# Performance work log

Hardware: AMD Instinct MI355X
Metric: run time of the kernel (lower is better)

The kernel has to match this reference:

```python
import jax, jax.numpy as jnp
import numpy as np

NUM_RBF = 16
MAX_REL = 32          # max_relative_feature
AUTOREGRESSIVE = True
D_MIN, D_MAX = 2.0, 22.0
LN_EPS = 1e-5


def setup_inputs() -> dict:
    key = jax.random.key(0)
    ks = jax.random.split(key, 6)
    B, L, A, K = 1, 1280, 14, 30
    E_feat, edge_in = 128, 16 + NUM_RBF * 4 * 10  # 656
    X = jax.random.normal(ks[0], (B, L, A, 3), dtype=jnp.float32) * 3.0
    residue_idx = jnp.tile(jnp.arange(L, dtype=jnp.int32)[None], (B, 1))
    chain_labels = jnp.zeros((B, L), dtype=jnp.int32)
    E_idx = jax.random.randint(ks[1], (B, L, K), 0, L, dtype=jnp.int32)
    atom_mask = jnp.ones((B, L, A), dtype=jnp.float32)
    W_pos = jax.random.normal(ks[2], (2 * MAX_REL + 2, 16), dtype=jnp.float32) * 0.1
    b_pos = jnp.zeros((16,), dtype=jnp.float32)
    W_edge = jax.random.normal(ks[3], (edge_in, E_feat), dtype=jnp.float32) * 0.05
    ln_gamma = jnp.ones((E_feat,), dtype=jnp.float32)
    ln_beta = jnp.zeros((E_feat,), dtype=jnp.float32)
    return {"X": X, "residue_idx": residue_idx, "chain_labels": chain_labels,
            "E_idx": E_idx, "atom_mask": atom_mask, "W_pos": W_pos,
            "b_pos": b_pos, "W_edge": W_edge, "ln_gamma": ln_gamma,
            "ln_beta": ln_beta}


def _forward(X, residue_idx, chain_labels, E_idx, W_pos, b_pos, W_edge,
             ln_gamma, ln_beta):
    B, L, A, _ = X.shape
    K = E_idx.shape[-1]
    # backbone atoms in loop order [Ca, N, C, O] -> X indices [1, 0, 2, 3]
    bb = X[:, :, jnp.array([1, 0, 2, 3]), :]          # [B, L, 4, 3]
    sc = X[:, :, 4:, :]                               # [B, L, 10, 3]
    Abb = jnp.transpose(bb, (0, 2, 1, 3))             # [B, 4, L, 3]
    Asc = jnp.transpose(sc, (0, 2, 1, 3))             # [B, 10, L, 3]
    # dense pairwise distances for all 40 (bb, sc) atom pairs: [B,4,10,L,L]
    diff = Abb[:, :, None, :, None, :] - Asc[:, None, :, None, :, :]
    D = jnp.sqrt(jnp.sum(diff * diff, axis=-1) + 1e-6)
    # gather top-k neighbor columns -> [B,4,10,L,K]
    D_nb = jnp.take_along_axis(D, E_idx[:, None, None, :, :], axis=4)
    mu = jnp.linspace(D_MIN, D_MAX, NUM_RBF, dtype=D_nb.dtype)
    sigma = (D_MAX - D_MIN) / NUM_RBF
    RBF = jnp.exp(-(((D_nb[..., None] - mu) / sigma) ** 2))  # [B,4,10,L,K,16]
    if AUTOREGRESSIVE:
        self_edges = (E_idx == jnp.arange(L, dtype=E_idx.dtype)[None, :, None])
        RBF = jnp.where(self_edges[:, None, None, :, :, None], 0.0, RBF)
    # concat order: bb outer, sc inner -> [B,L,K, 4*10*16]
    RBF_all = jnp.transpose(RBF, (0, 3, 4, 1, 2, 5)).reshape(B, L, K, 4 * 10 * NUM_RBF)
    # positional encodings
    offset = residue_idx[:, :, None] - residue_idx[:, None, :]        # [B,L,L]
    offset = jnp.take_along_axis(offset, E_idx, axis=2)               # [B,L,K]
    d_chains = (chain_labels[:, :, None] == chain_labels[:, None, :]).astype(jnp.int32)
    E_chains = jnp.take_along_axis(d_chains, E_idx, axis=2)           # [B,L,K]
    d = jnp.clip(offset + MAX_REL, 0, 2 * MAX_REL) * E_chains + (1 - E_chains) * (2 * MAX_REL + 1)
    d_onehot = jax.nn.one_hot(d, 2 * MAX_REL + 2, dtype=W_pos.dtype)  # [B,L,K,66]
    E_positional = d_onehot @ W_pos + b_pos                           # [B,L,K,16]
    E = jnp.concatenate([E_positional, RBF_all], axis=-1)             # [B,L,K,656]
    E = E @ W_edge                                                    # no bias
    # LayerNorm over last dim
    mean = jnp.mean(E, axis=-1, keepdims=True)
    var = jnp.mean((E - mean) ** 2, axis=-1, keepdims=True)
    E = (E - mean) / jnp.sqrt(var + LN_EPS) * ln_gamma + ln_beta
    return E


def reference(X, residue_idx, chain_labels, E_idx, atom_mask, W_pos, b_pos,
              W_edge, ln_gamma, ln_beta):
    E = _forward(X, residue_idx, chain_labels, E_idx, W_pos, b_pos, W_edge,
                 ln_gamma, ln_beta)
    return (E, E_idx)
```

## Files before the change

kernel.cpp:

```cpp
#include <hip/hip_runtime.h>

typedef short bf16x8 __attribute__((ext_vector_type(8)));
typedef float f32x4  __attribute__((ext_vector_type(4)));

#define L_RES 1280
#define A_ATM 14
#define K_NB  30
#define FEAT  656
#define KPAD  672
#define NKB   21
#define NCH   128
#define AF_STRIDE 680
#define EP_STRIDE 136
#define E_OUT_OFF (L_RES * K_NB * NCH)
#define NEDGE (L_RES * K_NB)

__device__ __forceinline__ ushort f2bf(float x) {
    union { float f; unsigned u; } v; v.f = x;
    unsigned r = (v.u + 0x7fffu + ((v.u >> 16) & 1u)) >> 16;
    return (ushort)r;
}

__global__ __launch_bounds__(256) void prep_kernel(const float* __restrict__ W,
                                                   const int* __restrict__ Eidx,
                                                   ushort* __restrict__ Wpack,
                                                   float* __restrict__ out) {
    const int blk = blockIdx.x;
    const int t = threadIdx.x;
    if (blk < 42) {
        int u = blk * 256 + t;
        if (u >= 84 * 128) return;
        int kbq = u >> 7;
        int n   = u & 127;
        int kb   = kbq >> 2;
        int quad = kbq & 3;
        ushort val[8];
#pragma unroll
        for (int j = 0; j < 8; j++) {
            int k = kb * 32 + quad * 8 + j;
            val[j] = (k < FEAT) ? f2bf(W[k * NCH + n]) : (ushort)0;
        }
        int lane = quad * 16 + (n & 15);
        ushort* dst = Wpack + (size_t)((((n >> 4) * NKB + kb) * 64 + lane) * 8);
        *(ulonglong2*)dst = *(const ulonglong2*)val;
    } else {
        int gid = (blk - 42) * 256 + t;
        if (gid < NEDGE) out[E_OUT_OFF + gid] = (float)Eidx[gid];
    }
}

__global__ __launch_bounds__(512) void sidechain_feat_kernel(
    const float* __restrict__ X,
    const int*   __restrict__ ridx,
    const int*   __restrict__ clab,
    const int*   __restrict__ Eidx,
    const float* __restrict__ Wpos,
    const float* __restrict__ bpos,
    const ushort* __restrict__ Wpack,
    const float* __restrict__ gamma,
    const float* __restrict__ beta,
    float* __restrict__ out)
{
    __shared__ __align__(16) ushort Af[64][AF_STRIDE];
    __shared__ float bbs[8][3];
    __shared__ float scj[2 * K_NB][10][3];
    __shared__ int   nbr[2 * K_NB];

    const int i0 = blockIdx.x * 2;
    const int t = threadIdx.x;
    const int w = t >> 6;
    const int lane = t & 63;

    if (t < 24) {
        const int perm[4] = {1, 0, 2, 3};
        int res = t / 12, r = t - res * 12;
        int a = r / 3, c = r - a * 3;
        bbs[res * 4 + a][c] = X[((i0 + res) * A_ATM + perm[a]) * 3 + c];
    }
    if (t < 2 * K_NB) nbr[t] = Eidx[i0 * K_NB + t];
    __syncthreads();

    for (int idx = t; idx < 2 * K_NB * 30; idx += 512) {
        int e = idx / 30;
        int r = idx - e * 30;
        int a = r / 3, c = r - a * 3;
        scj[e][a][c] = X[(nbr[e] * A_ATM + 4 + a) * 3 + c];
    }

    for (int idx = t; idx < 2 * K_NB * 16; idx += 512) {
        int e = idx >> 4, c = idx & 15;
        int res = i0 + (e >= K_NB);
        int row = e + (e >= K_NB ? 2 : 0);
        int j = nbr[e];
        int d;
        if (clab[res] == clab[j]) {
            int off = ridx[res] - ridx[j] + 32;
            d = off < 0 ? 0 : (off > 64 ? 64 : off);
        } else {
            d = 65;
        }
        Af[row][c] = f2bf(Wpos[d * 16 + c] + bpos[c]);
    }
    for (int idx = t; idx < 4 * AF_STRIDE; idx += 512) {
        int pr = idx / AF_STRIDE;
        int row = (pr & 1) + (pr >> 1) * 32 + 30;
        Af[row][idx % AF_STRIDE] = 0;
    }
    for (int idx = t; idx < 60 * 24; idx += 512) {
        int e = idx / 24;
        int row = e + (e >= K_NB ? 2 : 0);
        Af[row][FEAT + idx % 24] = 0;
    }
    __syncthreads();

    for (int idx = t; idx < 2 * K_NB * 40; idx += 512) {
        int e  = idx / 40;
        int p  = idx - e * 40;
        int ab = p / 10, as = p - ab * 10;
        int hi = (e >= K_NB);
        int row = e + hi * 2;
        float dx = bbs[hi * 4 + ab][0] - scj[e][as][0];
        float dy = bbs[hi * 4 + ab][1] - scj[e][as][1];
        float dz = bbs[hi * 4 + ab][2] - scj[e][as][2];
        float dist = sqrtf(dx * dx + dy * dy + dz * dz + 1e-6f);
        bool self = (nbr[e] == i0 + hi);
        unsigned* dst = (unsigned*)&Af[row][16 + p * 16];
#pragma unroll
        for (int q = 0; q < 8; q++) {
            float m0 = 2.0f + (float)(2 * q)     * (20.0f / 15.0f);
            float m1 = 2.0f + (float)(2 * q + 1) * (20.0f / 15.0f);
            float a0 = (dist - m0) * 0.8f;
            float a1 = (dist - m1) * 0.8f;
            float r0 = self ? 0.0f : __expf(-a0 * a0);
            float r1 = self ? 0.0f : __expf(-a1 * a1);
            dst[q] = (unsigned)f2bf(r0) | ((unsigned)f2bf(r1) << 16);
        }
    }
    __syncthreads();

    const int frow = lane & 15;
    const int quad = lane >> 4;
    const ushort* Ap[4];
#pragma unroll
    for (int m = 0; m < 4; m++) Ap[m] = &Af[m * 16 + frow][quad * 8];
    const ushort* Bp = Wpack + (size_t)((w * NKB) * 64 + lane) * 8;

    f32x4 acc[4];
#pragma unroll
    for (int m = 0; m < 4; m++) acc[m] = (f32x4){0.f, 0.f, 0.f, 0.f};

    bf16x8 a[4], b;
#pragma unroll
    for (int m = 0; m < 4; m++) a[m] = *(const bf16x8*)(Ap[m]);
    b = *(const bf16x8*)(Bp);

#pragma unroll
    for (int kb = 0; kb < NKB; kb++) {
        bf16x8 ca[4] = {a[0], a[1], a[2], a[3]};
        bf16x8 cb = b;
        if (kb + 1 < NKB) {
#pragma unroll
            for (int m = 0; m < 4; m++) a[m] = *(const bf16x8*)(Ap[m] + (kb + 1) * 32);
            b = *(const bf16x8*)(Bp + (size_t)(kb + 1) * 512);
        }
#pragma unroll
        for (int m = 0; m < 4; m++)
            acc[m] = __builtin_amdgcn_mfma_f32_16x16x32_bf16(ca[m], cb, acc[m], 0, 0, 0);
    }

    __syncthreads();
    float (*Epre)[EP_STRIDE] = (float (*)[EP_STRIDE])&Af[0][0];

#pragma unroll
    for (int m = 0; m < 4; m++)
#pragma unroll
        for (int r = 0; r < 4; r++)
            Epre[m * 16 + quad * 4 + r][w * 16 + frow] = acc[m][r];
    __syncthreads();

    for (int e = w; e < 2 * K_NB; e += 8) {
        int row = e + (e >= K_NB ? 2 : 0);
        float v0 = Epre[row][lane];
        float v1 = Epre[row][lane + 64];
        float s = v0 + v1;
        float q = v0 * v0 + v1 * v1;
#pragma unroll
        for (int off = 32; off > 0; off >>= 1) {
            s += __shfl_xor(s, off);
            q += __shfl_xor(q, off);
        }
        float mean = s * (1.0f / 128.0f);
        float var  = q * (1.0f / 128.0f) - mean * mean;
        float rstd = rsqrtf(var + 1e-5f);
        int eo = (e >= K_NB) ? (K_NB + e - K_NB) : e;
        float* o = out + (size_t)((i0 + (e >= K_NB)) * K_NB + (e % K_NB)) * NCH;
        (void)eo;
        o[lane]      = (v0 - mean) * rstd * gamma[lane]      + beta[lane];
        o[lane + 64] = (v1 - mean) * rstd * gamma[lane + 64] + beta[lane + 64];
    }
}

extern "C" void kernel_launch(void* const* d_in, const int* in_sizes, int n_in,
                              void* d_out, int out_size, void* d_ws, size_t ws_size,
                              hipStream_t stream) {
    const float* X     = (const float*)d_in[0];
    const int*   ridx  = (const int*)  d_in[1];
    const int*   clab  = (const int*)  d_in[2];
    const int*   Eidx  = (const int*)  d_in[3];
    const float* Wpos  = (const float*)d_in[5];
    const float* bpos  = (const float*)d_in[6];
    const float* Wedge = (const float*)d_in[7];
    const float* gamma = (const float*)d_in[8];
    const float* beta  = (const float*)d_in[9];
    float* out = (float*)d_out;

    ushort* Wpack = (ushort*)d_ws;

    prep_kernel<<<42 + (NEDGE + 255) / 256, 256, 0, stream>>>(Wedge, Eidx, Wpack, out);
    sidechain_feat_kernel<<<L_RES / 2, 512, 0, stream>>>(
        X, ridx, clab, Eidx, Wpos, bpos, Wpack, gamma, beta, out);
}
```

Measured before the change: 120.0 us.

## Build RBF A-fragments in registers per wave and drop shared-memory staging

The main kernel is restructured so that each wave owns one residue (32 padded edge rows) and computes all 128 output channels. The RBF and positional features are generated directly into MFMA A-operand registers, so the large shared-memory feature tile and most block barriers go away. LayerNorm is done in registers with 16-lane shuffles, and the E_idx copy moves from the prep kernel into the main kernel. In exchange, every wave re-reads all of the packed weights from global/L2 and holds 16 accumulators, which raises register pressure and lowers occupancy.

```diff
diff --git a/kernel.cpp b/kernel.cpp
--- a/kernel.cpp
+++ b/kernel.cpp
@@ -7,11 +7,9 @@
 #define A_ATM 14
 #define K_NB  30
 #define FEAT  656
-#define KPAD  672
 #define NKB   21
 #define NCH   128
-#define AF_STRIDE 680
-#define EP_STRIDE 136
+#define FRAG  512
 #define E_OUT_OFF (L_RES * K_NB * NCH)
 #define NEDGE (L_RES * K_NB)
 
@@ -22,34 +20,22 @@
 }
 
 __global__ __launch_bounds__(256) void prep_kernel(const float* __restrict__ W,
-                                                   const int* __restrict__ Eidx,
-                                                   ushort* __restrict__ Wpack,
-                                                   float* __restrict__ out) {
-    const int blk = blockIdx.x;
-    const int t = threadIdx.x;
-    if (blk < 42) {
-        int u = blk * 256 + t;
-        if (u >= 84 * 128) return;
-        int kbq = u >> 7;
-        int n   = u & 127;
-        int kb   = kbq >> 2;
-        int quad = kbq & 3;
-        ushort val[8];
-#pragma unroll
-        for (int j = 0; j < 8; j++) {
-            int k = kb * 32 + quad * 8 + j;
-            val[j] = (k < FEAT) ? f2bf(W[k * NCH + n]) : (ushort)0;
-        }
-        int lane = quad * 16 + (n & 15);
-        ushort* dst = Wpack + (size_t)((((n >> 4) * NKB + kb) * 64 + lane) * 8);
-        *(ulonglong2*)dst = *(const ulonglong2*)val;
-    } else {
-        int gid = (blk - 42) * 256 + t;
-        if (gid < NEDGE) out[E_OUT_OFF + gid] = (float)Eidx[gid];
-    }
-}
-
-__global__ __launch_bounds__(512) void sidechain_feat_kernel(
+                                                   ushort* __restrict__ Wpack) {
+    int u = blockIdx.x * 256 + threadIdx.x;
+    if (u >= 84 * 128) return;
+    int kbq = u >> 7, n = u & 127;
+    int kb = kbq >> 2, quad = kbq & 3;
+    ushort val[8];
+#pragma unroll
+    for (int j = 0; j < 8; j++) {
+        int k = kb * 32 + quad * 8 + j;
+        val[j] = (k < FEAT) ? f2bf(W[k * NCH + n]) : (ushort)0;
+    }
+    ushort* dst = Wpack + (size_t)((((n >> 4) * NKB + kb) * 64 + quad * 16 + (n & 15)) * 8);
+    *(ulonglong2*)dst = *(const ulonglong2*)val;
+}
+
+__global__ __launch_bounds__(256) void sidechain_fused_kernel(
     const float* __restrict__ X,
     const int*   __restrict__ ridx,
     const int*   __restrict__ clab,
@@ -61,142 +47,139 @@
     const float* __restrict__ beta,
     float* __restrict__ out)
 {
-    __shared__ __align__(16) ushort Af[64][AF_STRIDE];
-    __shared__ float bbs[8][3];
-    __shared__ float scj[2 * K_NB][10][3];
-    __shared__ int   nbr[2 * K_NB];
-
-    const int i0 = blockIdx.x * 2;
-    const int t = threadIdx.x;
-    const int w = t >> 6;
+    __shared__ float scj[4][K_NB][10][3];
+    __shared__ float bbs[4][4][3];
+
+    const int t    = threadIdx.x;
+    const int w    = t >> 6;
     const int lane = t & 63;
-
-    if (t < 24) {
-        const int perm[4] = {1, 0, 2, 3};
-        int res = t / 12, r = t - res * 12;
-        int a = r / 3, c = r - a * 3;
-        bbs[res * 4 + a][c] = X[((i0 + res) * A_ATM + perm[a]) * 3 + c];
-    }
-    if (t < 2 * K_NB) nbr[t] = Eidx[i0 * K_NB + t];
-    __syncthreads();
-
-    for (int idx = t; idx < 2 * K_NB * 30; idx += 512) {
-        int e = idx / 30;
-        int r = idx - e * 30;
-        int a = r / 3, c = r - a * 3;
-        scj[e][a][c] = X[(nbr[e] * A_ATM + 4 + a) * 3 + c];
-    }
-
-    for (int idx = t; idx < 2 * K_NB * 16; idx += 512) {
-        int e = idx >> 4, c = idx & 15;
-        int res = i0 + (e >= K_NB);
-        int row = e + (e >= K_NB ? 2 : 0);
-        int j = nbr[e];
-        int d;
-        if (clab[res] == clab[j]) {
-            int off = ridx[res] - ridx[j] + 32;
-            d = off < 0 ? 0 : (off > 64 ? 64 : off);
-        } else {
-            d = 65;
-        }
-        Af[row][c] = f2bf(Wpos[d * 16 + c] + bpos[c]);
-    }
-    for (int idx = t; idx < 4 * AF_STRIDE; idx += 512) {
-        int pr = idx / AF_STRIDE;
-        int row = (pr & 1) + (pr >> 1) * 32 + 30;
-        Af[row][idx % AF_STRIDE] = 0;
-    }
-    for (int idx = t; idx < 60 * 24; idx += 512) {
-        int e = idx / 24;
-        int row = e + (e >= K_NB ? 2 : 0);
-        Af[row][FEAT + idx % 24] = 0;
-    }
-    __syncthreads();
-
-    for (int idx = t; idx < 2 * K_NB * 40; idx += 512) {
-        int e  = idx / 40;
-        int p  = idx - e * 40;
-        int ab = p / 10, as = p - ab * 10;
-        int hi = (e >= K_NB);
-        int row = e + hi * 2;
-        float dx = bbs[hi * 4 + ab][0] - scj[e][as][0];
-        float dy = bbs[hi * 4 + ab][1] - scj[e][as][1];
-        float dz = bbs[hi * 4 + ab][2] - scj[e][as][2];
-        float dist = sqrtf(dx * dx + dy * dy + dz * dz + 1e-6f);
-        bool self = (nbr[e] == i0 + hi);
-        unsigned* dst = (unsigned*)&Af[row][16 + p * 16];
-#pragma unroll
-        for (int q = 0; q < 8; q++) {
-            float m0 = 2.0f + (float)(2 * q)     * (20.0f / 15.0f);
-            float m1 = 2.0f + (float)(2 * q + 1) * (20.0f / 15.0f);
-            float a0 = (dist - m0) * 0.8f;
-            float a1 = (dist - m1) * 0.8f;
-            float r0 = self ? 0.0f : __expf(-a0 * a0);
-            float r1 = self ? 0.0f : __expf(-a1 * a1);
-            dst[q] = (unsigned)f2bf(r0) | ((unsigned)f2bf(r1) << 16);
-        }
-    }
-    __syncthreads();
-
+    const int i    = blockIdx.x * 4 + w;
     const int frow = lane & 15;
     const int quad = lane >> 4;
-    const ushort* Ap[4];
-#pragma unroll
-    for (int m = 0; m < 4; m++) Ap[m] = &Af[m * 16 + frow][quad * 8];
-    const ushort* Bp = Wpack + (size_t)((w * NKB) * 64 + lane) * 8;
-
-    f32x4 acc[4];
-#pragma unroll
-    for (int m = 0; m < 4; m++) acc[m] = (f32x4){0.f, 0.f, 0.f, 0.f};
-
-    bf16x8 a[4], b;
-#pragma unroll
-    for (int m = 0; m < 4; m++) a[m] = *(const bf16x8*)(Ap[m]);
-    b = *(const bf16x8*)(Bp);
+
+    if (lane < 12) {
+        const int perm[4] = {1, 0, 2, 3};
+        int a = lane / 3, c = lane - a * 3;
+        bbs[w][a][c] = X[(i * A_ATM + perm[a]) * 3 + c];
+    }
+    for (int idx = lane; idx < K_NB * 30; idx += 64) {
+        int e = idx / 30, r = idx - e * 30;
+        int a = r / 3, c = r - a * 3;
+        int j = Eidx[i * K_NB + e];
+        scj[w][e][a][c] = X[(j * A_ATM + 4 + a) * 3 + c];
+    }
+    if (lane < K_NB) out[E_OUT_OFF + i * K_NB + lane] = (float)Eidx[i * K_NB + lane];
+
+    const int e0 = frow;
+    const int e1 = 16 + frow;
+    const bool v1 = (e1 < K_NB);
+    const int j0 = Eidx[i * K_NB + e0];
+    const int j1 = v1 ? Eidx[i * K_NB + e1] : 0;
+    const bool rbf0 = (j0 != i);
+    const bool rbf1 = v1 && (j1 != i);
+
+    const int ri = ridx[i], ci = clab[i];
+    int d0, d1;
+    {
+        int off0 = ri - ridx[j0] + 32;
+        off0 = off0 < 0 ? 0 : (off0 > 64 ? 64 : off0);
+        d0 = (ci == clab[j0]) ? off0 : 65;
+        int off1 = ri - ridx[j1] + 32;
+        off1 = off1 < 0 ? 0 : (off1 > 64 ? 64 : off1);
+        d1 = (ci == clab[j1]) ? off1 : 65;
+    }
+
+    const ushort* Bbase = Wpack + (size_t)lane * 8;
+    f32x4 acc0[8], acc1[8];
+#pragma unroll
+    for (int n = 0; n < 8; n++) {
+        acc0[n] = (f32x4){0.f, 0.f, 0.f, 0.f};
+        acc1[n] = (f32x4){0.f, 0.f, 0.f, 0.f};
+    }
 
 #pragma unroll
     for (int kb = 0; kb < NKB; kb++) {
-        bf16x8 ca[4] = {a[0], a[1], a[2], a[3]};
-        bf16x8 cb = b;
-        if (kb + 1 < NKB) {
-#pragma unroll
-            for (int m = 0; m < 4; m++) a[m] = *(const bf16x8*)(Ap[m] + (kb + 1) * 32);
-            b = *(const bf16x8*)(Bp + (size_t)(kb + 1) * 512);
+        bf16x8 b[8];
+#pragma unroll
+        for (int n = 0; n < 8; n++)
+            b[n] = *(const bf16x8*)(Bbase + (size_t)(n * NKB + kb) * FRAG);
+
+        ushort u0[8], u1[8];
+        if (kb == 0 && quad < 2) {
+#pragma unroll
+            for (int j = 0; j < 8; j++) {
+                int c = quad * 8 + j;
+                float bp = bpos[c];
+                u0[j] = f2bf(Wpos[d0 * 16 + c] + bp);
+                u1[j] = v1 ? f2bf(Wpos[d1 * 16 + c] + bp) : (ushort)0;
+            }
+        } else {
+            bool kv = !(kb == NKB - 1 && quad >= 2);
+            int p  = kv ? (2 * kb - 1 + (quad >> 1)) : 0;
+            int r0 = (quad & 1) * 8;
+            int ab = p / 10, as = p - ab * 10;
+            float bx = bbs[w][ab][0], by = bbs[w][ab][1], bz = bbs[w][ab][2];
+            float x0 = scj[w][e0][as][0], y0 = scj[w][e0][as][1], z0 = scj[w][e0][as][2];
+            int e1c = v1 ? e1 : 0;
+            float x1 = scj[w][e1c][as][0], y1 = scj[w][e1c][as][1], z1 = scj[w][e1c][as][2];
+            float dx0 = bx - x0, dy0 = by - y0, dz0 = bz - z0;
+            float dx1 = bx - x1, dy1 = by - y1, dz1 = bz - z1;
+            float dist0 = sqrtf(dx0 * dx0 + dy0 * dy0 + dz0 * dz0 + 1e-6f);
+            float dist1 = sqrtf(dx1 * dx1 + dy1 * dy1 + dz1 * dz1 + 1e-6f);
+            bool m0ok = kv && rbf0, m1ok = kv && rbf1;
+#pragma unroll
+            for (int j = 0; j < 8; j++) {
+                float mu = 2.0f + (float)(r0 + j) * (20.0f / 15.0f);
+                float t0 = (dist0 - mu) * 0.8f;
+                float t1 = (dist1 - mu) * 0.8f;
+                u0[j] = m0ok ? f2bf(__expf(-t0 * t0)) : (ushort)0;
+                u1[j] = m1ok ? f2bf(__expf(-t1 * t1)) : (ushort)0;
+            }
         }
-#pragma unroll
-        for (int m = 0; m < 4; m++)
-            acc[m] = __builtin_amdgcn_mfma_f32_16x16x32_bf16(ca[m], cb, acc[m], 0, 0, 0);
-    }
-
-    __syncthreads();
-    float (*Epre)[EP_STRIDE] = (float (*)[EP_STRIDE])&Af[0][0];
-
-#pragma unroll
-    for (int m = 0; m < 4; m++)
-#pragma unroll
-        for (int r = 0; r < 4; r++)
-            Epre[m * 16 + quad * 4 + r][w * 16 + frow] = acc[m][r];
-    __syncthreads();
-
-    for (int e = w; e < 2 * K_NB; e += 8) {
-        int row = e + (e >= K_NB ? 2 : 0);
-        float v0 = Epre[row][lane];
-        float v1 = Epre[row][lane + 64];
-        float s = v0 + v1;
-        float q = v0 * v0 + v1 * v1;
-#pragma unroll
-        for (int off = 32; off > 0; off >>= 1) {
-            s += __shfl_xor(s, off);
-            q += __shfl_xor(q, off);
+        bf16x8 a0 = *(const bf16x8*)u0;
+        bf16x8 a1 = *(const bf16x8*)u1;
+#pragma unroll
+        for (int n = 0; n < 8; n++)
+            acc0[n] = __builtin_amdgcn_mfma_f32_16x16x32_bf16(a0, b[n], acc0[n], 0, 0, 0);
+#pragma unroll
+        for (int n = 0; n < 8; n++)
+            acc1[n] = __builtin_amdgcn_mfma_f32_16x16x32_bf16(a1, b[n], acc1[n], 0, 0, 0);
+    }
+
+    float g[8], bt[8];
+#pragma unroll
+    for (int n = 0; n < 8; n++) {
+        g[n]  = gamma[n * 16 + frow];
+        bt[n] = beta[n * 16 + frow];
+    }
+
+#pragma unroll
+    for (int m = 0; m < 2; m++) {
+        f32x4* acc = m ? acc1 : acc0;
+#pragma unroll
+        for (int r = 0; r < 4; r++) {
+            float s = 0.f, q = 0.f;
+#pragma unroll
+            for (int n = 0; n < 8; n++) {
+                float v = acc[n][r];
+                s += v; q += v * v;
+            }
+#pragma unroll
+            for (int off = 1; off < 16; off <<= 1) {
+                s += __shfl_xor(s, off);
+                q += __shfl_xor(q, off);
+            }
+            float mean = s * (1.0f / 128.0f);
+            float var  = q * (1.0f / 128.0f) - mean * mean;
+            float rstd = rsqrtf(var + 1e-5f);
+            int edge = m * 16 + quad * 4 + r;
+            if (edge < K_NB) {
+                float* o = out + ((size_t)i * K_NB + edge) * NCH + frow;
+#pragma unroll
+                for (int n = 0; n < 8; n++)
+                    o[n * 16] = (acc[n][r] - mean) * rstd * g[n] + bt[n];
+            }
         }
-        float mean = s * (1.0f / 128.0f);
-        float var  = q * (1.0f / 128.0f) - mean * mean;
-        float rstd = rsqrtf(var + 1e-5f);
-        int eo = (e >= K_NB) ? (K_NB + e - K_NB) : e;
-        float* o = out + (size_t)((i0 + (e >= K_NB)) * K_NB + (e % K_NB)) * NCH;
-        (void)eo;
-        o[lane]      = (v0 - mean) * rstd * gamma[lane]      + beta[lane];
-        o[lane + 64] = (v1 - mean) * rstd * gamma[lane + 64] + beta[lane + 64];
     }
 }
 
@@ -216,7 +199,7 @@
 
     ushort* Wpack = (ushort*)d_ws;
 
-    prep_kernel<<<42 + (NEDGE + 255) / 256, 256, 0, stream>>>(Wedge, Eidx, Wpack, out);
-    sidechain_feat_kernel<<<L_RES / 2, 512, 0, stream>>>(
+    prep_kernel<<<42, 256, 0, stream>>>(Wedge, Wpack);
+    sidechain_fused_kernel<<<L_RES / 4, 256, 0, stream>>>(
         X, ridx, clab, Eidx, Wpos, bpos, Wpack, gamma, beta, out);
 }
```

Result: faster. 112.5 us (-6.3%).
